# Kernel optimization log

Measured on AMD Instinct MI355X. Metric: run time of the kernel, lower is better.

The kernel has to match this reference:

```python
import jax, jax.numpy as jnp
import numpy as np
import math
from functools import partial

PAD_IDX = 0
EPS = 1e-5  # torch LayerNorm default
H = 8       # num_heads

def _layernorm(x, g, b):
    m = x.mean(-1, keepdims=True)
    v = ((x - m) ** 2).mean(-1, keepdims=True)  # biased var, as torch LN
    return (x - m) / jnp.sqrt(v + EPS) * g + b

def setup_inputs() -> dict:
    key = jax.random.key(0)
    V, D, F, L, B, T = 32000, 512, 2048, 6, 8, 2048
    ks = jax.random.split(key, 24)
    n = lambda k, s: jax.random.normal(k, s, jnp.float32) * 0.02
    x = jax.random.randint(ks[0], (B, T), 1, V)
    x = x.at[:B // 2, -64:].set(PAD_IDX)  # padded tails to exercise mask
    embed = n(ks[1], (V, D)).at[PAD_IDX].set(0.0)  # padding_idx row is zero
    pos = np.arange(T)[:, None].astype(np.float32)
    div = np.exp(np.arange(0, D, 2).astype(np.float32) * (-math.log(10000.0) / D))
    pe = np.zeros((T, D), np.float32)
    pe[:, 0::2] = np.sin(pos * div)
    pe[:, 1::2] = np.cos(pos * div)
    # per-layer params stacked on leading L axis; Linear weights stored [in, out]
    return {
        'x': x, 'embed': embed, 'pe': jnp.asarray(pe),
        'Wq': n(ks[2], (L, D, D)), 'bq': jnp.zeros((L, D)),
        'Wk': n(ks[3], (L, D, D)), 'bk': jnp.zeros((L, D)),
        'Wv': n(ks[4], (L, D, D)), 'bv': jnp.zeros((L, D)),
        'Wo': n(ks[5], (L, D, D)), 'bo': jnp.zeros((L, D)),
        'ln1_g': jnp.ones((L, D)), 'ln1_b': jnp.zeros((L, D)),
        'W1': n(ks[6], (L, D, F)), 'b1': jnp.zeros((L, F)),
        'W2': n(ks[7], (L, F, D)), 'b2': jnp.zeros((L, D)),
        'ln2_g': jnp.ones((L, D)), 'ln2_b': jnp.zeros((L, D)),
        'sent_W': n(ks[8], (D, 3)), 'sent_b': jnp.zeros((3,)),
        'len_W': n(ks[9], (D, 3)), 'len_b': jnp.zeros((3,)),
    }

def reference(x, embed, pe, Wq, bq, Wk, bk, Wv, bv, Wo, bo, ln1_g, ln1_b,
              W1, b1, W2, b2, ln2_g, ln2_b, sent_W, sent_b, len_W, len_b):
    B, T = x.shape
    D = embed.shape[1]
    dk = D // H
    mask = (x == PAD_IDX)  # [B,T], True at pad keys
    h = embed[x] + pe[:T]  # [B,T,D]

    def block(h, p):
        wq, bq_, wk, bk_, wv, bv_, wo, bo_, g1, gb1, w1, fb1, w2, fb2, g2, gb2 = p
        q = (h @ wq + bq_).reshape(B, T, H, dk)
        k = (h @ wk + bk_).reshape(B, T, H, dk)
        v = (h @ wv + bv_).reshape(B, T, H, dk)
        scores = jnp.einsum('bqhd,bkhd->bhqk', q, k) / math.sqrt(dk)  # [B,H,T,T]
        scores = jnp.where(mask[:, None, None, :], -jnp.inf, scores)
        attn = jax.nn.softmax(scores, axis=-1)
        o = jnp.einsum('bhqk,bkhd->bqhd', attn, v).reshape(B, T, D) @ wo + bo_
        h = _layernorm(h + o, g1, gb1)
        ff = jax.nn.relu(h @ w1 + fb1) @ w2 + fb2
        h = _layernorm(h + ff, g2, gb2)
        return h, None

    params = (Wq, bq, Wk, bk, Wv, bv, Wo, bo, ln1_g, ln1_b, W1, b1, W2, b2, ln2_g, ln2_b)
    h, _ = jax.lax.scan(block, h, params)
    cls = h[:, 0, :]
    return (cls @ sent_W + sent_b, cls @ len_W + len_b, cls)
```

## Files before the change

### kernel.cpp

```cpp
#include <hip/hip_runtime.h>
#include <hip/hip_bf16.h>

typedef __bf16 bf16x8 __attribute__((ext_vector_type(8)));
typedef float f32x4 __attribute__((ext_vector_type(4)));
typedef float f32x16 __attribute__((ext_vector_type(16)));
typedef short s16x8 __attribute__((ext_vector_type(8)));
typedef unsigned u32x4 __attribute__((ext_vector_type(4)));

#define LOG2E 1.44269504088896f

__device__ __forceinline__ void gll16(const void* g, void* l) {
  __builtin_amdgcn_global_load_lds((const __attribute__((address_space(1))) void*)g,
                                   (__attribute__((address_space(3))) void*)l, 16, 0, 0);
}

__device__ __forceinline__ unsigned cvt_pk_bf16(float lo, float hi_) {
  unsigned r;
  asm("v_cvt_pk_bf16_f32 %0, %1, %2" : "=v"(r) : "v"(lo), "v"(hi_));
  return r;
}
__device__ __forceinline__ void pswap(unsigned& a, unsigned& b) {
  asm("v_permlane32_swap_b32 %0, %1" : "+v"(a), "+v"(b));
}

__device__ __forceinline__ int swzv(int row, int cbyte) {
  return (row * 128 + cbyte) ^ (((row >> 3) & 7) << 4);
}

__global__ __launch_bounds__(256)
void wtrans_kernel(const float* __restrict__ in, __hip_bfloat16* __restrict__ out,
                   int K, int N, size_t lstride_in, size_t lstride_out) {
  __shared__ float tile[64][65];
  const size_t mi = (size_t)blockIdx.z * lstride_in;
  const size_t mo = (size_t)blockIdx.z * lstride_out;
  const int k0 = blockIdx.x * 64, n0 = blockIdx.y * 64;
  const int t = threadIdx.x;
  const int r = t >> 4, c = (t & 15) * 4;
#pragma unroll
  for (int it = 0; it < 4; ++it) {
    const float4 v = *(const float4*)&in[mi + (size_t)(k0 + it * 16 + r) * N + n0 + c];
    tile[it * 16 + r][c + 0] = v.x; tile[it * 16 + r][c + 1] = v.y;
    tile[it * 16 + r][c + 2] = v.z; tile[it * 16 + r][c + 3] = v.w;
  }
  __syncthreads();
#pragma unroll
  for (int it = 0; it < 4; ++it) {
    const int n = it * 16 + r;
    __hip_bfloat16 hb[4];
#pragma unroll
    for (int j = 0; j < 4; ++j) hb[j] = __float2bfloat16(tile[c + j][n]);
    *(uint2*)&out[mo + (size_t)(n0 + n) * K + k0 + c] = *(uint2*)hb;
  }
}

__global__ void kbias_kernel(const int* __restrict__ x, float* __restrict__ kb) {
  const int i = blockIdx.x * 256 + threadIdx.x;
  kb[i] = (x[i] == 0) ? -1e30f : 0.f;
}

__global__ void tmask_kernel(const int* __restrict__ x, unsigned* __restrict__ tm) {
  const int tid = threadIdx.x;
  const int w = tid >> 6, lane = tid & 63;
  const int b = w * 2 + (lane >> 5), kt = lane & 31;
  int all64 = 1, any = 0;
  for (int i = 0; i < 64; ++i) {
    const int v = (x[b * 2048 + kt * 64 + i] == 0);
    any |= v; all64 &= v;
  }
  const unsigned long long bf = __ballot(all64);
  const unsigned long long bp = __ballot(any && !all64);
  if (lane == 0) { tm[(w * 2) * 2] = (unsigned)bf; tm[(w * 2) * 2 + 1] = (unsigned)bp; }
  if (lane == 32) { tm[(w * 2 + 1) * 2] = (unsigned)(bf >> 32); tm[(w * 2 + 1) * 2 + 1] = (unsigned)(bp >> 32); }
}

__global__ void bcat_kernel(const float* __restrict__ bq, const float* __restrict__ bk,
                            const float* __restrict__ bv, float* __restrict__ o) {
  const int l = blockIdx.x, t = threadIdx.x;
  o[l * 1536 + t] = bq[l * 512 + t];
  o[l * 1536 + 512 + t] = bk[l * 512 + t];
  o[l * 1536 + 1024 + t] = bv[l * 512 + t];
}

__global__ __launch_bounds__(128)
void embed_kernel(const int* __restrict__ x, const float* __restrict__ emb,
                  const float* __restrict__ pe, __hip_bfloat16* __restrict__ hbf) {
  const int row = blockIdx.x;
  const int t = row & 2047;
  const int tok = x[row];
  const int d = threadIdx.x * 4;
  const float4 e = *(const float4*)&emb[(size_t)tok * 512 + d];
  const float4 p = *(const float4*)&pe[(size_t)t * 512 + d];
  __hip_bfloat16 hb[4] = {__float2bfloat16(e.x + p.x), __float2bfloat16(e.y + p.y),
                          __float2bfloat16(e.z + p.z), __float2bfloat16(e.w + p.w)};
  *(uint2*)&hbf[(size_t)row * 512 + d] = *(uint2*)hb;
}

template <bool RELU, bool ADDRES>
__global__ __launch_bounds__(256, 4)
void gemm_kernel(const __hip_bfloat16* __restrict__ A, const __hip_bfloat16* __restrict__ Bt,
                 const float* __restrict__ bias, const __hip_bfloat16* __restrict__ res,
                 __hip_bfloat16* __restrict__ Cb, int M, int N, int K) {
  constexpr int BK = 32;
  __shared__ __hip_bfloat16 Ash[2][128 * BK];
  __shared__ __hip_bfloat16 Bsh[2][128 * BK];
  const int m0 = blockIdx.x * 128, n0 = blockIdx.y * 128;
  const int tid = threadIdx.x;
  const int lane = tid & 63, wid = tid >> 6;
  const int wr = wid >> 1, wc = wid & 1;
  const int cl = lane & 15, gr = lane >> 4;

  const int ar = tid >> 2;
  const int ac = (tid & 3) << 3;
  const __hip_bfloat16* Ag = A + (size_t)(m0 + ar) * K + ac;
  const __hip_bfloat16* Bg = Bt + (size_t)(n0 + ar) * K + ac;
  const int ldst = tid * 8;

  f32x4 acc[4][4] = {};
  const int KT = K / BK;

  auto stage = [&](int buf, int kt) {
    const size_t ko = (size_t)kt * BK;
    gll16(Ag + ko, &Ash[buf][ldst]);
    gll16(Ag + ko + (size_t)64 * K, &Ash[buf][2048 + ldst]);
    gll16(Bg + ko, &Bsh[buf][ldst]);
    gll16(Bg + ko + (size_t)64 * K, &Bsh[buf][2048 + ldst]);
  };

  stage(0, 0);
  __syncthreads();
  int cur = 0;
  for (int kt = 0; kt < KT; ++kt) {
    if (kt + 1 < KT) stage(cur ^ 1, kt + 1);
    bf16x8 aF[4], bF[4];
#pragma unroll
    for (int i = 0; i < 4; ++i) {
      aF[i] = *(const bf16x8*)&Ash[cur][(wr * 64 + i * 16 + cl) * BK + gr * 8];
      bF[i] = *(const bf16x8*)&Bsh[cur][(wc * 64 + i * 16 + cl) * BK + gr * 8];
    }
#pragma unroll
    for (int i = 0; i < 4; ++i)
#pragma unroll
      for (int j = 0; j < 4; ++j)
        acc[i][j] = __builtin_amdgcn_mfma_f32_16x16x32_bf16(aF[i], bF[j], acc[i][j], 0, 0, 0);
    __syncthreads();
    cur ^= 1;
  }

  float bv[4];
#pragma unroll
  for (int j = 0; j < 4; ++j) bv[j] = bias[n0 + wc * 64 + j * 16 + cl];
#pragma unroll
  for (int i = 0; i < 4; ++i) {
    const int rowb = m0 + wr * 64 + i * 16 + gr * 4;
#pragma unroll
    for (int rr = 0; rr < 4; ++rr) {
      const size_t ro = (size_t)(rowb + rr) * N;
#pragma unroll
      for (int j = 0; j < 4; ++j) {
        float v = acc[i][j][rr] + bv[j];
        const int col = n0 + wc * 64 + j * 16 + cl;
        if (ADDRES) v += __bfloat162float(res[ro + col]);
        if (RELU) v = v > 0.f ? v : 0.f;
        Cb[ro + col] = __float2bfloat16(v);
      }
    }
  }
}

__global__ __launch_bounds__(256)
void vtrans_kernel(const __hip_bfloat16* __restrict__ qkv, __hip_bfloat16* __restrict__ vt) {
  constexpr int T = 2048, QS = 1536;
  __shared__ __hip_bfloat16 tile[64 * 64];
  const int tt = blockIdx.x, bh = blockIdx.y;
  const int b = bh >> 3, h = bh & 7;
  const int tid = threadIdx.x;
  const int r = tid >> 2, c0 = (tid & 3) * 16;
  const __hip_bfloat16* src = qkv + ((size_t)(b * T + tt * 64 + r)) * QS + 1024 + h * 64 + c0;
  *(bf16x8*)((char*)tile + swzv(r, c0 * 2)) = *(const bf16x8*)src;
  *(bf16x8*)((char*)tile + swzv(r, c0 * 2 + 16)) = *(const bf16x8*)(src + 8);
  __syncthreads();
  __hip_bfloat16 buf[16];
#pragma unroll
  for (int j = 0; j < 16; ++j)
    buf[j] = *(__hip_bfloat16*)((char*)tile + swzv(c0 + j, r * 2));
  __hip_bfloat16* dst = vt + ((size_t)(bh * 64 + r)) * T + tt * 64 + c0;
  *(uint4*)dst = ((uint4*)buf)[0];
  *(uint4*)(dst + 8) = ((uint4*)buf)[1];
}

__global__ __launch_bounds__(512, 2)
void attn9_kernel(const __hip_bfloat16* __restrict__ qkv, const __hip_bfloat16* __restrict__ Vt,
                  const float* __restrict__ kbias, const unsigned* __restrict__ tmaskg,
                  __hip_bfloat16* __restrict__ Og) {
  constexpr int T = 2048, NT = T / 64, QS = 1536;
  __shared__ __hip_bfloat16 Ks[2][64 * 64];
  __shared__ __hip_bfloat16 Vs[2][64 * 64];
  __shared__ float bc[8][32];
  const int bid = blockIdx.x;
  const int wg = (bid & 7) * 64 + (bid >> 3);
  const int qb = wg & 7, bh = wg >> 3;
  const int b = bh >> 3, h = bh & 7;
  const int tid = threadIdx.x;
  const int w = tid >> 6, lane = tid & 63;
  const int col = lane & 31, hi = lane >> 5;
  const unsigned fullm = tmaskg[b * 2], partm = tmaskg[b * 2 + 1];

  const int sr = tid >> 3;
  const int sc = 8 * ((tid & 7) ^ (sr & 7));
  const __hip_bfloat16* kp = qkv + ((size_t)(b * T + sr)) * QS + 512 + h * 64 + sc;
  const __hip_bfloat16* vp = Vt + ((size_t)(bh * 64 + sr)) * T + sc;

  auto stage = [&](int buf, int kt) {
    gll16(kp + (size_t)kt * 64 * QS, (char*)Ks[buf] + tid * 16);
    gll16(vp + kt * 64, (char*)Vs[buf] + tid * 16);
  };

  const float qscale = 0.125f * LOG2E;
  s16x8 qf[4];
  {
    const __hip_bfloat16* qptr =
        qkv + ((size_t)(b * T + qb * 256 + w * 32 + col)) * QS + h * 64 + 8 * hi;
#pragma unroll
    for (int ks = 0; ks < 4; ++ks) {
      s16x8 raw = *(const s16x8*)(qptr + ks * 16);
#pragma unroll
      for (int j = 0; j < 8; ++j) {
        const unsigned u = ((unsigned)(unsigned short)raw[j]) << 16;
        const float f = __uint_as_float(u) * qscale;
        const __hip_bfloat16 hb = __float2bfloat16(f);
        raw[j] = *(const short*)&hb;
      }
      qf[ks] = raw;
    }
  }

  stage(0, 0);
  __syncthreads();

  f32x16 o0 = {}, o1 = {};
  f32x4 lacc = {};

  for (int kt = 0; kt < NT; ++kt) {
    const int cur = kt & 1;
    if (kt + 1 < NT) stage(cur ^ 1, kt + 1);

    if (!((fullm >> kt) & 1)) {
      const char* kbase = (const char*)Ks[cur];
      const char* vbase = (const char*)Vs[cur];
      const bool part = (partm >> kt) & 1;
      const float* kbp = kbias + (size_t)b * T + kt * 64;

#pragma unroll
      for (int kb2 = 0; kb2 < 2; ++kb2) {
        f32x16 s = {};
        {
          const char* khalf = kbase + kb2 * 4096;
          __builtin_amdgcn_s_setprio(1);
#pragma unroll
          for (int ks = 0; ks < 4; ++ks) {
            const int sl = ((2 * ks + hi) ^ (col & 7)) * 16;
            const bf16x8 k8 = *(const bf16x8*)(khalf + col * 128 + sl);
            s = __builtin_amdgcn_mfma_f32_32x32x16_bf16(k8, *(const bf16x8*)&qf[ks], s, 0, 0, 0);
          }
          __builtin_amdgcn_s_setprio(0);
        }

        if (part) {
#pragma unroll
          for (int r = 0; r < 16; ++r) {
            const int k16 = (r & 3) + 8 * (r >> 2) + 4 * hi;
            s[r] += kbp[kb2 * 32 + k16];
          }
        }

#pragma unroll
        for (int r = 0; r < 16; ++r) {
          s[r] = __builtin_amdgcn_exp2f(s[r]);
          lacc[r & 3] += s[r];
        }

#pragma unroll
        for (int half = 0; half < 2; ++half) {
          const int ks = kb2 * 2 + half;
          const int rb = half * 8;
          unsigned wa = cvt_pk_bf16(s[rb + 0], s[rb + 1]);
          unsigned wb = cvt_pk_bf16(s[rb + 2], s[rb + 3]);
          unsigned wc = cvt_pk_bf16(s[rb + 4], s[rb + 5]);
          unsigned wd = cvt_pk_bf16(s[rb + 6], s[rb + 7]);
          pswap(wa, wc);
          pswap(wb, wd);
          const u32x4 paw = {wa, wb, wc, wd};
          const bf16x8 pa = __builtin_bit_cast(bf16x8, paw);
          const int sl = ((2 * ks + hi) ^ (col & 7)) * 16;
          const bf16x8 v0 = *(const bf16x8*)(vbase + col * 128 + sl);
          const bf16x8 v1 = *(const bf16x8*)(vbase + 4096 + col * 128 + sl);
          __builtin_amdgcn_s_setprio(1);
          o0 = __builtin_amdgcn_mfma_f32_32x32x16_bf16(pa, v0, o0, 0, 0, 0);
          o1 = __builtin_amdgcn_mfma_f32_32x32x16_bf16(pa, v1, o1, 0, 0, 0);
          __builtin_amdgcn_s_setprio(0);
        }
      }
    }
    __syncthreads();
  }

  float sm[4];
#pragma unroll
  for (int r = 0; r < 4; ++r) sm[r] = lacc[r];
  sm[0] += sm[2]; sm[1] += sm[3]; sm[0] += sm[1];
  const float lrun = sm[0] + __shfl_xor(sm[0], 32);

  bc[w][col] = 1.f / lrun;
  __hip_bfloat16* op = Og + ((size_t)(b * T + qb * 256 + w * 32)) * 512 + h * 64;
#pragma unroll
  for (int r = 0; r < 16; ++r) {
    const int query = (r & 3) + 8 * (r >> 2) + 4 * hi;
    const float li = bc[w][query];
    op[(size_t)query * 512 + col] = __float2bfloat16(o0[r] * li);
    op[(size_t)query * 512 + 32 + col] = __float2bfloat16(o1[r] * li);
  }
}

__global__ __launch_bounds__(128)
void ln_kernel(const __hip_bfloat16* __restrict__ in, const float* __restrict__ g,
               const float* __restrict__ be, __hip_bfloat16* __restrict__ hbf) {
  const int row = blockIdx.x;
  const int tid = threadIdx.x;
  const int d = tid * 4;
  __shared__ float red[4];
  const size_t off = (size_t)row * 512 + d;
  const uint2 pu = *(const uint2*)&in[off];
  const __hip_bfloat16* ph = (const __hip_bfloat16*)&pu;
  float a[4];
#pragma unroll
  for (int j = 0; j < 4; ++j) a[j] = __bfloat162float(ph[j]);
  float s = a[0] + a[1] + a[2] + a[3];
  float q = a[0] * a[0] + a[1] * a[1] + a[2] * a[2] + a[3] * a[3];
#pragma unroll
  for (int o2 = 1; o2 < 64; o2 <<= 1) {
    s += __shfl_xor(s, o2);
    q += __shfl_xor(q, o2);
  }
  const int w = tid >> 6;
  if ((tid & 63) == 0) { red[w * 2] = s; red[w * 2 + 1] = q; }
  __syncthreads();
  s = red[0] + red[2]; q = red[1] + red[3];
  const float mean = s * (1.f / 512.f);
  const float var = q * (1.f / 512.f) - mean * mean;
  const float rstd = rsqrtf(var + 1e-5f);
  const float4 gg = *(const float4*)&g[d];
  const float4 bb = *(const float4*)&be[d];
  __hip_bfloat16 hb[4] = {
      __float2bfloat16((a[0] - mean) * rstd * gg.x + bb.x),
      __float2bfloat16((a[1] - mean) * rstd * gg.y + bb.y),
      __float2bfloat16((a[2] - mean) * rstd * gg.z + bb.z),
      __float2bfloat16((a[3] - mean) * rstd * gg.w + bb.w)};
  *(uint2*)&hbf[off] = *(uint2*)hb;
}

__global__ __launch_bounds__(256)
void head_kernel(const __hip_bfloat16* __restrict__ hbf, const float* __restrict__ sW,
                 const float* __restrict__ sb, const float* __restrict__ lW,
                 const float* __restrict__ lb, float* __restrict__ out) {
  const int tid = threadIdx.x;
  for (int i = tid; i < 4096; i += 256) {
    const int bb = i >> 9, d = i & 511;
    out[48 + i] = __bfloat162float(hbf[(size_t)bb * 2048 * 512 + d]);
  }
  if (tid < 192) {
    const int g = tid >> 2, s4 = tid & 3;
    const int which = g / 24, rem = g % 24;
    const int bb = rem / 3, j = rem % 3;
    const float* W = which ? lW : sW;
    const float* bias = which ? lb : sb;
    const __hip_bfloat16* cls = hbf + (size_t)bb * 2048 * 512;
    float acc = 0.f;
    for (int d = s4; d < 512; d += 4) acc += __bfloat162float(cls[d]) * W[d * 3 + j];
    acc += __shfl_xor(acc, 1);
    acc += __shfl_xor(acc, 2);
    if (s4 == 0) out[which * 24 + bb * 3 + j] = acc + bias[j];
  }
}

extern "C" void kernel_launch(void* const* d_in, const int* in_sizes, int n_in,
                              void* d_out, int out_size, void* d_ws, size_t ws_size,
                              hipStream_t stream) {
  (void)in_sizes; (void)n_in; (void)out_size; (void)ws_size;
  const int* x = (const int*)d_in[0];
  const float* embed = (const float*)d_in[1];
  const float* pe = (const float*)d_in[2];
  const float* Wq = (const float*)d_in[3];
  const float* bq = (const float*)d_in[4];
  const float* Wk = (const float*)d_in[5];
  const float* bk = (const float*)d_in[6];
  const float* Wv = (const float*)d_in[7];
  const float* bvv = (const float*)d_in[8];
  const float* Wo = (const float*)d_in[9];
  const float* bo = (const float*)d_in[10];
  const float* ln1g = (const float*)d_in[11];
  const float* ln1b = (const float*)d_in[12];
  const float* W1 = (const float*)d_in[13];
  const float* b1 = (const float*)d_in[14];
  const float* W2 = (const float*)d_in[15];
  const float* b2 = (const float*)d_in[16];
  const float* ln2g = (const float*)d_in[17];
  const float* ln2b = (const float*)d_in[18];
  const float* sW = (const float*)d_in[19];
  const float* sb = (const float*)d_in[20];
  const float* lW = (const float*)d_in[21];
  const float* lb = (const float*)d_in[22];
  float* out = (float*)d_out;

  constexpr int L = 6, Dm = 512, F = 2048, B = 8, T = 2048;
  constexpr int M = B * T;
  constexpr int QS = 1536;

  char* w = (char*)d_ws;
  auto alloc = [&](size_t bytes) {
    char* p = w; w += (bytes + 255) & ~(size_t)255; return p;
  };
  __hip_bfloat16* wqkvt = (__hip_bfloat16*)alloc((size_t)L * QS * Dm * 2);
  __hip_bfloat16* wot = (__hip_bfloat16*)alloc((size_t)L * Dm * Dm * 2);
  __hip_bfloat16* w1t = (__hip_bfloat16*)alloc((size_t)L * Dm * F * 2);
  __hip_bfloat16* w2t = (__hip_bfloat16*)alloc((size_t)L * Dm * F * 2);
  float* bqkv = (float*)alloc((size_t)L * QS * 4);
  __hip_bfloat16* hbf = (__hip_bfloat16*)alloc((size_t)M * Dm * 2);
  char* regionA = alloc((size_t)M * F * 2);
  __hip_bfloat16* vtg = (__hip_bfloat16*)regionA;
  __hip_bfloat16* attno = (__hip_bfloat16*)(regionA + (size_t)M * Dm * 2);
  __hip_bfloat16* ffn1 = (__hip_bfloat16*)regionA;
  char* regionB = alloc((size_t)M * QS * 2);
  __hip_bfloat16* qkvb = (__hip_bfloat16*)regionB;
  __hip_bfloat16* tmpb = (__hip_bfloat16*)regionB;
  float* kbias = (float*)alloc((size_t)M * 4);
  unsigned* tmask = (unsigned*)alloc(64);

  const size_t DD = (size_t)Dm * Dm;
  wtrans_kernel<<<dim3(8, 8, L), 256, 0, stream>>>(Wq, wqkvt, Dm, Dm, DD, (size_t)QS * Dm);
  wtrans_kernel<<<dim3(8, 8, L), 256, 0, stream>>>(Wk, wqkvt + DD, Dm, Dm, DD, (size_t)QS * Dm);
  wtrans_kernel<<<dim3(8, 8, L), 256, 0, stream>>>(Wv, wqkvt + 2 * DD, Dm, Dm, DD, (size_t)QS * Dm);
  wtrans_kernel<<<dim3(8, 8, L), 256, 0, stream>>>(Wo, wot, Dm, Dm, DD, DD);
  wtrans_kernel<<<dim3(8, 32, L), 256, 0, stream>>>(W1, w1t, Dm, F, (size_t)Dm * F, (size_t)Dm * F);
  wtrans_kernel<<<dim3(32, 8, L), 256, 0, stream>>>(W2, w2t, F, Dm, (size_t)Dm * F, (size_t)Dm * F);
  bcat_kernel<<<L, 512, 0, stream>>>(bq, bk, bvv, bqkv);
  kbias_kernel<<<M / 256, 256, 0, stream>>>(x, kbias);
  tmask_kernel<<<1, 256, 0, stream>>>(x, tmask);
  embed_kernel<<<M, 128, 0, stream>>>(x, embed, pe, hbf);

  for (int l = 0; l < L; ++l) {
    const __hip_bfloat16* wqkv_ = wqkvt + (size_t)l * QS * Dm;
    const __hip_bfloat16* wo_ = wot + (size_t)l * Dm * Dm;
    const __hip_bfloat16* w1_ = w1t + (size_t)l * Dm * F;
    const __hip_bfloat16* w2_ = w2t + (size_t)l * Dm * F;

    gemm_kernel<false, false><<<dim3(128, 12), 256, 0, stream>>>(hbf, wqkv_, bqkv + l * QS, nullptr, qkvb, M, QS, Dm);
    vtrans_kernel<<<dim3(32, 64), 256, 0, stream>>>(qkvb, vtg);
    attn9_kernel<<<512, 512, 0, stream>>>(qkvb, vtg, kbias, tmask, attno);
    gemm_kernel<false, true><<<dim3(128, 4), 256, 0, stream>>>(attno, wo_, bo + l * Dm, hbf, tmpb, M, Dm, Dm);
    ln_kernel<<<M, 128, 0, stream>>>(tmpb, ln1g + l * Dm, ln1b + l * Dm, hbf);
    gemm_kernel<true, false><<<dim3(128, 16), 256, 0, stream>>>(hbf, w1_, b1 + l * F, nullptr, ffn1, M, F, Dm);
    gemm_kernel<false, true><<<dim3(128, 4), 256, 0, stream>>>(ffn1, w2_, b2 + l * Dm, hbf, tmpb, M, Dm, F);
    ln_kernel<<<M, 128, 0, stream>>>(tmpb, ln2g + l * Dm, ln2b + l * Dm, hbf);
  }
  head_kernel<<<1, 256, 0, stream>>>(hbf, sW, sb, lW, lb, out);
}
```

Baseline: 1.494 ms.

## Add 256x256-tile GEMM kernel for QKV and FFN1 projections

```diff
diff --git a/kernel.cpp b/kernel.cpp
--- a/kernel.cpp
+++ b/kernel.cpp
@@ -161,6 +161,93 @@
         const int col = n0 + wc * 64 + j * 16 + cl;
         if (ADDRES) v += __bfloat162float(res[ro + col]);
         if (RELU) v = v > 0.f ? v : 0.f;
+        Cb[ro + col] = __float2bfloat16(v);
+      }
+    }
+  }
+}
+
+template <bool RELU>
+__global__ __launch_bounds__(512, 2)
+void gemm256_kernel(const __hip_bfloat16* __restrict__ A, const __hip_bfloat16* __restrict__ Bt,
+                    const float* __restrict__ bias, __hip_bfloat16* __restrict__ Cb,
+                    int M, int N, int K) {
+  __shared__ char smem[131072];
+  const int tid = threadIdx.x;
+  const int lane = tid & 63, wid = tid >> 6;
+  const int wr = wid >> 2, wc = wid & 3;
+  const int cl = lane & 15, gr = lane >> 4;
+  const int m0 = blockIdx.x * 256, n0 = blockIdx.y * 256;
+  const int swz16 = (gr ^ ((cl >> 1) & 3)) * 16;
+
+  const int sr1 = tid >> 2;
+  const int sc1 = (((tid & 3) ^ ((sr1 >> 1) & 3))) * 8;
+  const __hip_bfloat16* Ag1 = A + (size_t)(m0 + sr1) * K + sc1;
+  const __hip_bfloat16* Ag2 = A + (size_t)(m0 + sr1 + 128) * K + sc1;
+  const __hip_bfloat16* Bg1 = Bt + (size_t)(n0 + sr1) * K + sc1;
+  const __hip_bfloat16* Bg2 = Bt + (size_t)(n0 + sr1 + 128) * K + sc1;
+
+  auto stage = [&](int buf, int kt, int p) {
+    const size_t ko = (size_t)kt * 64 + p * 32;
+    char* ab = smem + buf * 65536 + p * 16384;
+    char* bb2 = ab + 32768;
+    gll16(Ag1 + ko, ab + tid * 16);
+    gll16(Ag2 + ko, ab + 8192 + tid * 16);
+    gll16(Bg1 + ko, bb2 + tid * 16);
+    gll16(Bg2 + ko, bb2 + 8192 + tid * 16);
+  };
+
+  f32x4 acc[8][4] = {};
+  const int KT = K / 64;
+
+  stage(0, 0, 0);
+  stage(0, 0, 1);
+
+  for (int kt = 0; kt < KT; ++kt) {
+    const char* abuf = smem + (kt & 1) * 65536;
+#pragma unroll
+    for (int p = 0; p < 2; ++p) {
+      if (kt == KT - 1 && p == 1) {
+        asm volatile("s_waitcnt vmcnt(0)" ::: "memory");
+      } else {
+        asm volatile("s_waitcnt vmcnt(4)" ::: "memory");
+      }
+      __builtin_amdgcn_s_barrier();
+      asm volatile("" ::: "memory");
+      if (kt + 1 < KT) stage((kt & 1) ^ 1, kt + 1, p);
+      const char* ah = abuf + p * 16384;
+      const char* bh = abuf + 32768 + p * 16384;
+      bf16x8 aF[8], bF[4];
+#pragma unroll
+      for (int i = 0; i < 8; ++i)
+        aF[i] = *(const bf16x8*)(ah + (wr * 128 + i * 16 + cl) * 64 + swz16);
+#pragma unroll
+      for (int j = 0; j < 4; ++j)
+        bF[j] = *(const bf16x8*)(bh + (wc * 64 + j * 16 + cl) * 64 + swz16);
+      __builtin_amdgcn_s_setprio(1);
+#pragma unroll
+      for (int i = 0; i < 8; ++i)
+#pragma unroll
+        for (int j = 0; j < 4; ++j)
+          acc[i][j] = __builtin_amdgcn_mfma_f32_16x16x32_bf16(aF[i], bF[j], acc[i][j], 0, 0, 0);
+      __builtin_amdgcn_s_setprio(0);
+    }
+  }
+
+  float bv[4];
+#pragma unroll
+  for (int j = 0; j < 4; ++j) bv[j] = bias[n0 + wc * 64 + j * 16 + cl];
+#pragma unroll
+  for (int i = 0; i < 8; ++i) {
+    const int rowb = m0 + wr * 128 + i * 16 + gr * 4;
+#pragma unroll
+    for (int rr = 0; rr < 4; ++rr) {
+      const size_t ro = (size_t)(rowb + rr) * N;
+#pragma unroll
+      for (int j = 0; j < 4; ++j) {
+        float v = acc[i][j][rr] + bv[j];
+        if (RELU) v = v > 0.f ? v : 0.f;
+        const int col = n0 + wc * 64 + j * 16 + cl;
         Cb[ro + col] = __float2bfloat16(v);
       }
     }
@@ -453,12 +540,12 @@
     const __hip_bfloat16* w1_ = w1t + (size_t)l * Dm * F;
     const __hip_bfloat16* w2_ = w2t + (size_t)l * Dm * F;
 
-    gemm_kernel<false, false><<<dim3(128, 12), 256, 0, stream>>>(hbf, wqkv_, bqkv + l * QS, nullptr, qkvb, M, QS, Dm);
+    gemm256_kernel<false><<<dim3(64, 6), 512, 0, stream>>>(hbf, wqkv_, bqkv + l * QS, qkvb, M, QS, Dm);
     vtrans_kernel<<<dim3(32, 64), 256, 0, stream>>>(qkvb, vtg);
     attn9_kernel<<<512, 512, 0, stream>>>(qkvb, vtg, kbias, tmask, attno);
     gemm_kernel<false, true><<<dim3(128, 4), 256, 0, stream>>>(attno, wo_, bo + l * Dm, hbf, tmpb, M, Dm, Dm);
     ln_kernel<<<M, 128, 0, stream>>>(tmpb, ln1g + l * Dm, ln1b + l * Dm, hbf);
-    gemm_kernel<true, false><<<dim3(128, 16), 256, 0, stream>>>(hbf, w1_, b1 + l * F, nullptr, ffn1, M, F, Dm);
+    gemm256_kernel<true><<<dim3(64, 8), 512, 0, stream>>>(hbf, w1_, b1 + l * F, ffn1, M, F, Dm);
     gemm_kernel<false, true><<<dim3(128, 4), 256, 0, stream>>>(ffn1, w2_, b2 + l * Dm, hbf, tmpb, M, Dm, F);
     ln_kernel<<<M, 128, 0, stream>>>(tmpb, ln2g + l * Dm, ln2b + l * Dm, hbf);
   }
```

Result: no change. 1.506 ms (+0.8%).
